# Kernel tuning notes

Hardware: AMD Instinct MI355X
Metric: run time of the kernel (lower is better)

The kernel has to match this reference:

```python
import jax, jax.numpy as jnp
import numpy as np

B = 1024; PAST = 64; FUT = 16; N = PAST + FUT; DM = N // 3; HID = 64
EMB = [(2000, 32), (7, 8), (24, 8)]
OUTP = 3 + 32 + 8 + 8  # 51 = out_preprocess
O = OUTP - 1           # 50
HID1 = 64; HID2 = 64
NEG = -1e30  # finite stand-in for -inf so fully-masked rows stay NaN-free


def _gcnn(x, A, W, act):
    # D = diag((1 + rowsum(sign(relu(A-1e-15))))^-0.5); out = act(D @ A @ D @ (x W^T))
    d = (1.0 + (A > 1e-15).astype(x.dtype).sum(1)) ** -0.5
    An = d[:, None] * A * d[None, :]            # (P,P)
    h = jnp.einsum('pq,bqc->bpc', An, x @ W.T)  # (B,P,out)
    return jax.nn.relu(h) if act else h


def _forward(data, emb0, emb1, emb2, w1, b1, w2, b2, w3, b3,
             M, Wg1a, Wg1b, Wk, smoothing, Wg2a, Wg2b):
    # learned adjacency: masked softmax over strictly-lower-triangular support
    mask = jnp.tril(jnp.ones((N, N), data.dtype), -1)
    A0 = jax.nn.relu(M @ M.T)
    A = jax.nn.softmax(jnp.where(mask > 0, A0, NEG), axis=1)
    A = jnp.where(mask > 0, A, 0.0)
    # pre_processing: embeddings + MLP, then re-append last raw column
    tabs = (emb0, emb1, emb2)
    e = [t[data[:, :, i].astype(jnp.int32)] for i, t in enumerate(tabs)]
    h = jnp.concatenate(e + [data[:, :, -3:]], -1)        # (B,N,51)
    h = jax.nn.relu(h @ w1.T + b1)
    h = jax.nn.relu(h @ w2.T + b2)
    h = h @ w3.T + b3                                      # (B,N,50)
    x = jnp.concatenate([h, data[:, :, -1:]], -1)          # (B,N,51)
    sg1, sg2 = x[:, :PAST], x[:, PAST:]
    A11 = A[:PAST, :PAST]
    x1 = _gcnn(_gcnn(sg1, A11, Wg1a, True), A11, Wg1b, False)   # (B,PAST,50)
    xk = jnp.concatenate([x1, sg2[:, :, :-1]], 1)               # (B,N,50)
    y = x[:, :PAST, -1:]                                        # (B,PAST,1)
    # Kernel: batched Mahalanobis quadratic form (diagonal computed directly)
    xp, xf = xk[:, :PAST], xk[:, PAST:]
    theta = Wk @ Wk.T
    theta = (theta + theta.T) / 2
    diff = xp[:, None, :, :] - xf[:, :, None, :]                # (B,F,P,50)
    q = jnp.einsum('bjip,pq,bjiq->bji', diff, theta, diff)      # (B,F,P)
    alpha = -0.5 * q / (jax.nn.sigmoid(smoothing[0]) * 0.01)
    At = A[FUT:, :PAST] if False else A[PAST:, :PAST]           # (F,P)
    At = jax.nn.softmax(jnp.where(At != 0, At, NEG), axis=1)
    # torch Softmax(dim=1) on (B,F,P) normalizes over the F axis
    alpha = jax.nn.softmax(jnp.where(At[None] >= 0.004, alpha, NEG), axis=1)
    yh = jnp.einsum('bjp,bpo->bjo', alpha, y)                   # (B,F,1)
    x2 = jnp.concatenate([sg2[:, :, :-1], yh], -1)              # (B,F,51)
    A22 = A[PAST:, PAST:]
    out = _gcnn(_gcnn(x2, A22, Wg2a, True), A22, Wg2b, False).reshape(-1, FUT)
    # cdist(x, x), p=2, with NaN-safe sqrt at zero distance
    xc = jnp.concatenate([sg1, x2], 1)                          # (B,N,51)
    sq = jnp.sum(xc * xc, -1)
    d2 = jnp.maximum(sq[:, :, None] + sq[:, None, :]
                     - 2.0 * jnp.einsum('bnc,bmc->bnm', xc, xc), 0.0)
    dist = jnp.where(d2 > 0, jnp.sqrt(jnp.where(d2 > 0, d2, 1.0)), 0.0)
    return (out, dist, A)


def setup_inputs() -> dict:
    key = jax.random.key(0)
    ks = jax.random.split(key, 20)
    cols = [jax.random.randint(ks[i], (B, N, 1), 0, EMB[i][0]).astype(jnp.float32)
            for i in range(3)]
    data = jnp.concatenate(cols + [jax.random.normal(ks[3], (B, N, 3), jnp.float32)], -1)
    g = lambda k, s, sc: jax.random.normal(k, s, jnp.float32) * sc
    return dict(
        data=data,
        emb0=g(ks[4], EMB[0], 1.0),
        emb1=g(ks[5], EMB[1], 1.0),
        emb2=g(ks[6], EMB[2], 1.0),
        w1=g(ks[7], (128, OUTP), OUTP ** -0.5), b1=jnp.zeros((128,), jnp.float32),
        w2=g(ks[8], (128, 128), 128 ** -0.5), b2=jnp.zeros((128,), jnp.float32),
        w3=g(ks[9], (O, 128), 128 ** -0.5), b3=jnp.zeros((O,), jnp.float32),
        M=g(ks[10], (N, DM), 1.0),
        Wg1a=g(ks[11], (HID1, OUTP), OUTP ** -0.5),
        Wg1b=g(ks[12], (O, HID1), HID1 ** -0.5),
        Wk=g(ks[13], (O, HID), 0.05),
        smoothing=g(ks[14], (1,), 1.0),
        Wg2a=g(ks[15], (HID2, OUTP), OUTP ** -0.5),
        Wg2b=g(ks[16], (1, HID2), HID2 ** -0.5),
    )


def reference(data, emb0, emb1, emb2, w1, b1, w2, b2, w3, b3,
              M, Wg1a, Wg1b, Wk, smoothing, Wg2a, Wg2b):
    return _forward(data, emb0, emb1, emb2, w1, b1, w2, b2, w3, b3,
                    M, Wg1a, Wg1b, Wk, smoothing, Wg2a, Wg2b)
```

## Files before the change

### kernel.cpp

```cpp
#include <hip/hip_runtime.h>
#include <math.h>


#define NEGBIG (-1e30f)

#define OFF_A     7471104
#define OFF_AN22  7481600
#define OFF_MK    7484356
#define OFF_GAH   7514692
#define OFF_GAL   7516740
#define OFF_G2AT  7521156
#define OFF_SC    7524420
#define OFF_W1H   7524424
#define OFF_W1L   7528520
#define OFF_W2H   7532616
#define OFF_W2L   7540808
#define OFF_W3H   7549000
#define OFF_W3L   7553096
#define OFF_ANH   7557192
#define OFF_ANL   7559240
#define OFF_GBH   7561288
#define OFF_GBL   7563336
#define OFF_WKH   7565384
#define OFF_WKL   7567432

#define OUT_OUT   0
#define OUT_DIST  16384
#define OUT_A     6569984

typedef __attribute__((ext_vector_type(8))) short bf16x8;
typedef __attribute__((ext_vector_type(4))) short s16x4;
typedef __attribute__((ext_vector_type(4))) float f32x4;

__device__ __forceinline__ unsigned short f2bf(float x) {
  union { float f; unsigned u; } v; v.f = x;
  unsigned r = v.u + 0x7fffu + ((v.u >> 16) & 1u);
  return (unsigned short)(r >> 16);
}
__device__ __forceinline__ float bf2f(unsigned short h) {
  union { unsigned u; float f; } v; v.u = ((unsigned)h) << 16; return v.f;
}
__device__ __forceinline__ void split2(float v, unsigned short& h, unsigned short& l) {
  unsigned short hh = f2bf(v);
  h = hh;
  l = f2bf(v - bf2f(hh));
}
__device__ __forceinline__ void split8(const float* v, bf16x8& h8, bf16x8& l8) {
#pragma unroll
  for (int j = 0; j < 8; ++j) {
    unsigned short hh, ll; split2(v[j], hh, ll);
    h8[j] = (short)hh; l8[j] = (short)ll;
  }
}
#define SWZ6(r, k) (((r) << 6) + (((((k) >> 3) ^ ((r) & 7)) << 3) | ((k) & 7)))
#define SWZ7(r, k) (((r) << 7) + (((((k) >> 3) ^ ((r) & 7)) << 3) | ((k) & 7)))

#define MFMA3(acc, aH, aL, bH, bL) \
  acc = __builtin_amdgcn_mfma_f32_16x16x32_bf16(aH, bH, acc, 0, 0, 0); \
  acc = __builtin_amdgcn_mfma_f32_16x16x32_bf16(aH, bL, acc, 0, 0, 0); \
  acc = __builtin_amdgcn_mfma_f32_16x16x32_bf16(aL, bH, acc, 0, 0, 0);
#define MFMA4(acc, aH, aL, bH, bL) \
  MFMA3(acc, aH, aL, bH, bL) \
  acc = __builtin_amdgcn_mfma_f32_16x16x32_bf16(aL, bL, acc, 0, 0, 0);

__global__ __launch_bounds__(256) void k_prep(
    const float* __restrict__ M, const float* __restrict__ Wk,
    const float* __restrict__ sm,
    const float* __restrict__ w1, const float* __restrict__ w2,
    const float* __restrict__ w3,
    const float* __restrict__ wg1a, const float* __restrict__ wg1b,
    const float* __restrict__ wg2a,
    float* __restrict__ ws, float* __restrict__ out)
{
  __shared__ float Msh[80 * 26];
  __shared__ float Ash[80 * 80];
  __shared__ float d1[64];
  __shared__ float d2s[16];
  const int t = threadIdx.x;

  if (blockIdx.x == 0) {
    for (int e = t; e < 80 * 26; e += 256) Msh[e] = M[e];
    __syncthreads();
    for (int e = t; e < 6400; e += 256) {
      int i = e / 80, j = e % 80;
      float v = 0.f;
      if (j < i) {
        float s = 0.f;
        for (int k = 0; k < 26; ++k) s += Msh[i * 26 + k] * Msh[j * 26 + k];
        v = s > 0.f ? s : 0.f;
      }
      Ash[e] = v;
    }
    __syncthreads();
    if (t > 0 && t < 80) {
      int i = t;
      float m = -3.4e38f;
      for (int j = 0; j < i; ++j) m = fmaxf(m, Ash[i * 80 + j]);
      float s = 0.f;
      for (int j = 0; j < i; ++j) {
        float e = expf(Ash[i * 80 + j] - m);
        Ash[i * 80 + j] = e;
        s += e;
      }
      float inv = 1.f / s;
      for (int j = 0; j < i; ++j) Ash[i * 80 + j] *= inv;
    }
    __syncthreads();
    {
      float* Aws = ws + OFF_A;
      float* Aout = out + OUT_A;
      for (int e = t; e < 6400; e += 256) { Aws[e] = Ash[e]; Aout[e] = Ash[e]; }
    }
    if (t < 64) {
      int c = 0;
      for (int j = 0; j < 64; ++j) if (Ash[t * 80 + j] > 1e-15f) ++c;
      d1[t] = 1.f / sqrtf(1.f + (float)c);
    } else if (t < 80) {
      int i = t - 64; int c = 0;
      for (int j = 0; j < 16; ++j) if (Ash[(64 + i) * 80 + 64 + j] > 1e-15f) ++c;
      d2s[i] = 1.f / sqrtf(1.f + (float)c);
    }
    __syncthreads();
    {
      float* an22 = ws + OFF_AN22;
      unsigned short* anH = (unsigned short*)(ws + OFF_ANH);
      unsigned short* anL = (unsigned short*)(ws + OFF_ANL);
      for (int e = t; e < 4096; e += 256) {
        int i = e >> 6, j = e & 63;
        float v = d1[i] * Ash[i * 80 + j] * d1[j];
        unsigned short h = f2bf(v);
        anH[e] = h; anL[e] = f2bf(v - bf2f(h));
      }
      for (int e = t; e < 256; e += 256) {
        int i = e >> 4, j = e & 15;
        an22[e] = d2s[i] * Ash[(64 + i) * 80 + 64 + j] * d2s[j];
      }
    }
    if (t < 16) {
      float* mk = ws + OFF_MK;
      int j = t;
      float m = -3.4e38f;
      for (int i = 0; i < 64; ++i) {
        float v = Ash[(64 + j) * 80 + i];
        v = (v != 0.f) ? v : NEGBIG;
        m = fmaxf(m, v);
      }
      float s = 0.f;
      for (int i = 0; i < 64; ++i) {
        float v = Ash[(64 + j) * 80 + i];
        v = (v != 0.f) ? v : NEGBIG;
        s += expf(v - m);
      }
      float inv = 1.f / s;
      for (int i = 0; i < 64; ++i) {
        float v = Ash[(64 + j) * 80 + i];
        v = (v != 0.f) ? v : NEGBIG;
        mk[j * 64 + i] = (expf(v - m) * inv >= 0.004f) ? 1.f : 0.f;
      }
    }
  } else if (blockIdx.x == 1) {
    unsigned short* wkh = (unsigned short*)(ws + OFF_WKH);
    unsigned short* wkl = (unsigned short*)(ws + OFF_WKL);
    for (int e = t; e < 4096; e += 256) {
      int h = e >> 6, o = e & 63;
      float v = (o < 50) ? Wk[o * 64 + h] : 0.f;
      unsigned short hh = f2bf(v);
      wkh[e] = hh; wkl[e] = f2bf(v - bf2f(hh));
    }
    if (t == 0) {
      float v = sm[0];
      float sig = 1.f / (1.f + expf(-v));
      (ws + OFF_SC)[0] = -0.5f / (sig * 0.01f);
    }
  } else if (blockIdx.x == 2) {
    unsigned short* w1h = (unsigned short*)(ws + OFF_W1H);
    unsigned short* w1l = (unsigned short*)(ws + OFF_W1L);
    for (int e = t; e < 8192; e += 256) {
      int n = e >> 6, k = e & 63;
      float v = (k < 51) ? w1[n * 51 + k] : 0.f;
      unsigned short h = f2bf(v);
      w1h[e] = h; w1l[e] = f2bf(v - bf2f(h));
    }
    unsigned short* w3h = (unsigned short*)(ws + OFF_W3H);
    unsigned short* w3l = (unsigned short*)(ws + OFF_W3L);
    for (int e = t; e < 8192; e += 256) {
      int n = e >> 7, k = e & 127;
      float v = (n < 50) ? w3[n * 128 + k] : 0.f;
      unsigned short h = f2bf(v);
      w3h[e] = h; w3l[e] = f2bf(v - bf2f(h));
    }
    unsigned short* gah = (unsigned short*)(ws + OFF_GAH);
    unsigned short* gal = (unsigned short*)(ws + OFF_GAL);
    for (int e = t; e < 4096; e += 256) {
      int n = e >> 6, k = e & 63;
      float v = (k < 51) ? wg1a[n * 51 + k] : 0.f;
      unsigned short h = f2bf(v);
      gah[e] = h; gal[e] = f2bf(v - bf2f(h));
    }
  } else {
    unsigned short* w2h = (unsigned short*)(ws + OFF_W2H);
    unsigned short* w2l = (unsigned short*)(ws + OFF_W2L);
    for (int e = t; e < 16384; e += 256) {
      int n = e >> 7, k = e & 127;
      float v = w2[n * 128 + k];
      unsigned short h = f2bf(v);
      w2h[e] = h; w2l[e] = f2bf(v - bf2f(h));
    }
    unsigned short* gbh = (unsigned short*)(ws + OFF_GBH);
    unsigned short* gbl = (unsigned short*)(ws + OFF_GBL);
    for (int e = t; e < 4096; e += 256) {
      int n = e >> 6, k = e & 63;
      float v = (n < 50) ? wg1b[n * 64 + k] : 0.f;
      unsigned short h = f2bf(v);
      gbh[e] = h; gbl[e] = f2bf(v - bf2f(h));
    }
    float* g2at = ws + OFF_G2AT;
    for (int e = t; e < 64 * 51; e += 256) { int o = e / 51, k = e % 51; g2at[k * 64 + o] = wg2a[e]; }
  }
}

__global__ __launch_bounds__(512, 4) void k_fused(
    const float* __restrict__ data,
    const float* __restrict__ emb0, const float* __restrict__ emb1,
    const float* __restrict__ emb2,
    const float* __restrict__ b1v, const float* __restrict__ b2v,
    const float* __restrict__ b3v,
    const float* __restrict__ wg2b,
    float* __restrict__ ws, float* __restrict__ out)
{
  __shared__ __align__(16) unsigned short SH[27136];

  unsigned short* xcH = SH;
  unsigned short* xcL = SH + 5120;
  unsigned short* b1H = SH + 10240;
  unsigned short* b1L = SH + 14336;
  unsigned short* b2H = SH + 18432;
  unsigned short* b2L = SH + 22528;
  float* spH2 = (float*)(SH + 26624);
  float* spS  = (float*)(SH + 26880);
  float* sfS  = (float*)(SH + 27008);
  float* yhsS = (float*)(SH + 27040);
  float* alS = (float*)(SH + 18432);
  unsigned short* zfH = SH + 22528;
  unsigned short* zfL = SH + 23552;
  unsigned short* mHdH = SH + 10240;
  unsigned short* mHdL = SH + 16384;
  float* X2v  = (float*)(SH + 10240);
  float* A22v = (float*)(SH + 11904);
  float* G2v  = (float*)(SH + 12416);
  float* Pmv  = (float*)(SH + 14464);
  float* wb2  = (float*)(SH + 16512);
  float* zzv  = (float*)(SH + 16640);
  float* sqS  = (float*)(SH + 16672);

  const int t = threadIdx.x, b = blockIdx.x;
  const int lane = t & 63, wave = t >> 6;
  const int m16 = lane & 15, quad = lane >> 4;
  const int s = wave & 3, half = wave >> 2;
  const int row0 = s * 16;
  const int arow = row0 + m16;

  const unsigned short* w1h = (const unsigned short*)(ws + OFF_W1H);
  const unsigned short* w1l = (const unsigned short*)(ws + OFF_W1L);
  const unsigned short* w2h = (const unsigned short*)(ws + OFF_W2H);
  const unsigned short* w2l = (const unsigned short*)(ws + OFF_W2L);
  const unsigned short* w3h = (const unsigned short*)(ws + OFF_W3H);
  const unsigned short* w3l = (const unsigned short*)(ws + OFF_W3L);
  const float* mk = ws + OFF_MK;
  const float* an22 = ws + OFF_AN22;
  const float* g2at = ws + OFF_G2AT;
  const unsigned short* gAnH = (const unsigned short*)(ws + OFF_ANH);
  const unsigned short* gAnL = (const unsigned short*)(ws + OFF_ANL);
  const unsigned short* gaH = (const unsigned short*)(ws + OFF_GAH);
  const unsigned short* gaL = (const unsigned short*)(ws + OFF_GAL);
  const unsigned short* gbH = (const unsigned short*)(ws + OFF_GBH);
  const unsigned short* gbL = (const unsigned short*)(ws + OFF_GBL);
  const unsigned short* gwkH = (const unsigned short*)(ws + OFF_WKH);
  const unsigned short* gwkL = (const unsigned short*)(ws + OFF_WKL);
  const float sc = (ws + OFF_SC)[0];

#pragma unroll
  for (int ck = 0; ck < 2; ++ck) {
    const int C0 = ck ? 48 : 0;
    const int NT = ck ? 2 : 3;

    {
      const int col = wave * 16 + m16;
      const float bias = b1v[col];
      f32x4 acc1[3];
#pragma unroll
      for (int rt = 0; rt < 3; ++rt) acc1[rt] = (f32x4){0.f, 0.f, 0.f, 0.f};
#pragma unroll
      for (int kh = 0; kh < 2; ++kh) {
        bf16x8 bH = *(const bf16x8*)(w1h + (col << 6) + kh * 32 + (quad << 3));
        bf16x8 bL = *(const bf16x8*)(w1l + (col << 6) + kh * 32 + (quad << 3));
#pragma unroll
        for (int rt = 0; rt < 3; ++rt) {
          if (rt >= NT) break;
          const int g = b * 80 + C0 + rt * 16 + m16;
          float v[8];
          if (kh == 0) {
            int i0 = (int)data[g * 6 + 0];
            const float* p = emb0 + i0 * 32 + (quad << 3);
#pragma unroll
            for (int j = 0; j < 8; ++j) v[j] = p[j];
          } else {
            if (quad == 0) {
              int i1 = (int)data[g * 6 + 1];
#pragma unroll
              for (int j = 0; j < 8; ++j) v[j] = emb1[i1 * 8 + j];
            } else if (quad == 1) {
              int i2 = (int)data[g * 6 + 2];
#pragma unroll
              for (int j = 0; j < 8; ++j) v[j] = emb2[i2 * 8 + j];
            } else if (quad == 2) {
              v[0] = data[g * 6 + 3]; v[1] = data[g * 6 + 4]; v[2] = data[g * 6 + 5];
#pragma unroll
              for (int j = 3; j < 8; ++j) v[j] = 0.f;
            } else {
#pragma unroll
              for (int j = 0; j < 8; ++j) v[j] = 0.f;
            }
          }
          bf16x8 aH, aL;
          split8(v, aH, aL);
          MFMA3(acc1[rt], aH, aL, bH, bL)
        }
      }
#pragma unroll
      for (int rt = 0; rt < 3; ++rt) {
        if (rt >= NT) break;
#pragma unroll
        for (int r = 0; r < 4; ++r) {
          float v = acc1[rt][r] + bias; v = v > 0.f ? v : 0.f;
          int idx = SWZ7(rt * 16 + quad * 4 + r, col);
          split2(v, mHdH[idx], mHdL[idx]);
        }
      }
    }
    __syncthreads();

    f32x4 acc2[3];
#pragma unroll
    for (int rt = 0; rt < 3; ++rt) acc2[rt] = (f32x4){0.f, 0.f, 0.f, 0.f};
    {
      const int col = wave * 16 + m16;
#pragma unroll
      for (int kh = 0; kh < 2; ++kh) {
        bf16x8 bh0 = *(const bf16x8*)(w2h + (col << 7) + ((quad + kh * 8) << 3));
        bf16x8 bl0 = *(const bf16x8*)(w2l + (col << 7) + ((quad + kh * 8) << 3));
        bf16x8 bh1 = *(const bf16x8*)(w2h + (col << 7) + ((quad + kh * 8 + 4) << 3));
        bf16x8 bl1 = *(const bf16x8*)(w2l + (col << 7) + ((quad + kh * 8 + 4) << 3));
#pragma unroll
        for (int lrt = 0; lrt < 3; ++lrt) {
          if (lrt >= NT) break;
          const int lr = lrt * 16 + m16;
          int ach0 = ((quad + kh * 8) ^ (m16 & 7)) << 3;
          int ach1 = ((quad + kh * 8 + 4) ^ (m16 & 7)) << 3;
          bf16x8 aH = *(const bf16x8*)(mHdH + (lr << 7) + ach0);
          bf16x8 aL = *(const bf16x8*)(mHdL + (lr << 7) + ach0);
          MFMA3(acc2[lrt], aH, aL, bh0, bl0)
          aH = *(const bf16x8*)(mHdH + (lr << 7) + ach1);
          aL = *(const bf16x8*)(mHdL + (lr << 7) + ach1);
          MFMA3(acc2[lrt], aH, aL, bh1, bl1)
        }
      }
    }
    __syncthreads();

    {
      const int col = wave * 16 + m16;
      const float bias = b2v[col];
#pragma unroll
      for (int lrt = 0; lrt < 3; ++lrt) {
        if (lrt >= NT) break;
#pragma unroll
        for (int r = 0; r < 4; ++r) {
          float v = acc2[lrt][r] + bias; v = v > 0.f ? v : 0.f;
          int idx = SWZ7(lrt * 16 + quad * 4 + r, col);
          split2(v, mHdH[idx], mHdL[idx]);
        }
      }
    }
    __syncthreads();

    {
      const int colt = wave & 3, rh = wave >> 2;
      const int col = colt * 16 + m16;
      const float bias = (col < 50) ? b3v[col] : 0.f;
      for (int lrt = rh; lrt < NT; lrt += 2) {
        const int lr = lrt * 16 + m16;
        f32x4 acc = (f32x4){0.f, 0.f, 0.f, 0.f};
#pragma unroll
        for (int kh = 0; kh < 2; ++kh) {
          bf16x8 bh0 = *(const bf16x8*)(w3h + (col << 7) + ((quad + kh * 8) << 3));
          bf16x8 bl0 = *(const bf16x8*)(w3l + (col << 7) + ((quad + kh * 8) << 3));
          bf16x8 bh1 = *(const bf16x8*)(w3h + (col << 7) + ((quad + kh * 8 + 4) << 3));
          bf16x8 bl1 = *(const bf16x8*)(w3l + (col << 7) + ((quad + kh * 8 + 4) << 3));
          int ach0 = ((quad + kh * 8) ^ (m16 & 7)) << 3;
          int ach1 = ((quad + kh * 8 + 4) ^ (m16 & 7)) << 3;
          bf16x8 aH = *(const bf16x8*)(mHdH + (lr << 7) + ach0);
          bf16x8 aL = *(const bf16x8*)(mHdL + (lr << 7) + ach0);
          MFMA3(acc, aH, aL, bh0, bl0)
          aH = *(const bf16x8*)(mHdH + (lr << 7) + ach1);
          aL = *(const bf16x8*)(mHdL + (lr << 7) + ach1);
          MFMA3(acc, aH, aL, bh1, bl1)
        }
        if (col != 50) {
#pragma unroll
          for (int r = 0; r < 4; ++r) {
            int grow = C0 + lrt * 16 + quad * 4 + r;
            int idx = SWZ6(grow, col);
            split2(acc[r] + bias, xcH[idx], xcL[idx]);
          }
        }
      }
      if (ck == 0 && t < 80) {
        float v = (t < 64) ? data[(b * 80 + t) * 6 + 5] : 0.f;
        int idx = SWZ6(t, 50);
        split2(v, xcH[idx], xcL[idx]);
      }
    }
    __syncthreads();
  }

  f32x4 accA[2];

#pragma unroll
  for (int n = 0; n < 2; ++n) accA[n] = (f32x4){0.f, 0.f, 0.f, 0.f};
#pragma unroll
  for (int kb8 = 0; kb8 < 8; kb8 += 4) {
    int ach = ((quad + kb8) ^ (m16 & 7)) << 3;
    int k0 = (quad + kb8) << 3;
    bf16x8 aH = *(const bf16x8*)(xcH + (arow << 6) + ach);
    bf16x8 aL = *(const bf16x8*)(xcL + (arow << 6) + ach);
#pragma unroll
    for (int n = 0; n < 2; ++n) {
      const int col = (half * 2 + n) * 16 + m16;
      bf16x8 bH = *(const bf16x8*)(gaH + (col << 6) + k0);
      bf16x8 bL = *(const bf16x8*)(gaL + (col << 6) + k0);
      MFMA3(accA[n], aH, aL, bH, bL)
    }
  }
  {
    const int kb = row0 + quad * 4;
#pragma unroll
    for (int n = 0; n < 2; ++n) {
      const int col = (half * 2 + n) * 16 + m16;
      int idx = (col << 6) + (((((kb >> 3) ^ (col & 7)) << 3)) | (kb & 7));
      s16x4 hv, lv;
#pragma unroll
      for (int r = 0; r < 4; ++r) {
        unsigned short hh, ll; split2(accA[n][r], hh, ll);
        hv[r] = (short)hh; lv[r] = (short)ll;
      }
      *(s16x4*)(b2H + idx) = hv; *(s16x4*)(b2L + idx) = lv;
    }
  }
  __syncthreads();

#pragma unroll
  for (int n = 0; n < 2; ++n) accA[n] = (f32x4){0.f, 0.f, 0.f, 0.f};
#pragma unroll
  for (int kb8 = 0; kb8 < 8; kb8 += 4) {
    int ach = ((quad + kb8) ^ (m16 & 7)) << 3;
    int k0 = (quad + kb8) << 3;
    bf16x8 aH = *(const bf16x8*)(gAnH + (arow << 6) + k0);
    bf16x8 aL = *(const bf16x8*)(gAnL + (arow << 6) + k0);
#pragma unroll
    for (int n = 0; n < 2; ++n) {
      const int col = (half * 2 + n) * 16 + m16;
      int boff = (col << 6) + ach;
      bf16x8 bH = *(const bf16x8*)(b2H + boff);
      bf16x8 bL = *(const bf16x8*)(b2L + boff);
      MFMA3(accA[n], aH, aL, bH, bL)
    }
  }
  __syncthreads();

  {
    const int kb = row0 + quad * 4;
#pragma unroll
    for (int n = 0; n < 2; ++n) {
      const int col = (half * 2 + n) * 16 + m16;
      int idx = (col << 6) + (((((kb >> 3) ^ (col & 7)) << 3)) | (kb & 7));
      s16x4 hv, lv;
#pragma unroll
      for (int r = 0; r < 4; ++r) {
        float v = accA[n][r]; v = v > 0.f ? v : 0.f;
        unsigned short hh, ll; split2(v, hh, ll);
        hv[r] = (short)hh; lv[r] = (short)ll;
      }
      *(s16x4*)(b2H + idx) = hv; *(s16x4*)(b2L + idx) = lv;
    }
  }
  __syncthreads();

#pragma unroll
  for (int n = 0; n < 2; ++n) accA[n] = (f32x4){0.f, 0.f, 0.f, 0.f};
#pragma unroll
  for (int kb8 = 0; kb8 < 8; kb8 += 4) {
    int ach = ((quad + kb8) ^ (m16 & 7)) << 3;
    int k0 = (quad + kb8) << 3;
    bf16x8 aH = *(const bf16x8*)(gAnH + (arow << 6) + k0);
    bf16x8 aL = *(const bf16x8*)(gAnL + (arow << 6) + k0);
#pragma unroll
    for (int n = 0; n < 2; ++n) {
      const int col = (half * 2 + n) * 16 + m16;
      int boff = (col << 6) + ach;
      bf16x8 bH = *(const bf16x8*)(b2H + boff);
      bf16x8 bL = *(const bf16x8*)(b2L + boff);
      MFMA3(accA[n], aH, aL, bH, bL)
    }
  }
#pragma unroll
  for (int n = 0; n < 2; ++n) {
    const int col = (half * 2 + n) * 16 + m16;
#pragma unroll
    for (int r = 0; r < 4; ++r) {
      int idx = SWZ6(row0 + quad * 4 + r, col);
      split2(accA[n][r], b1H[idx], b1L[idx]);
    }
  }
  __syncthreads();

#pragma unroll
  for (int n = 0; n < 2; ++n) accA[n] = (f32x4){0.f, 0.f, 0.f, 0.f};
#pragma unroll
  for (int kb8 = 0; kb8 < 8; kb8 += 4) {
    int ach = ((quad + kb8) ^ (m16 & 7)) << 3;
    int k0 = (quad + kb8) << 3;
    bf16x8 aH = *(const bf16x8*)(b1H + (arow << 6) + ach);
    bf16x8 aL = *(const bf16x8*)(b1L + (arow << 6) + ach);
#pragma unroll
    for (int n = 0; n < 2; ++n) {
      const int col = (half * 2 + n) * 16 + m16;
      bf16x8 bH = *(const bf16x8*)(gbH + (col << 6) + k0);
      bf16x8 bL = *(const bf16x8*)(gbL + (col << 6) + k0);
      MFMA3(accA[n], aH, aL, bH, bL)
    }
  }
#pragma unroll
  for (int n = 0; n < 2; ++n) {
    const int col = (half * 2 + n) * 16 + m16;
#pragma unroll
    for (int r = 0; r < 4; ++r) {
      int idx = SWZ6(row0 + quad * 4 + r, col);
      split2(accA[n][r], b2H[idx], b2L[idx]);
    }
  }
  __syncthreads();

#pragma unroll
  for (int n = 0; n < 2; ++n) accA[n] = (f32x4){0.f, 0.f, 0.f, 0.f};
  f32x4 af = (f32x4){0.f, 0.f, 0.f, 0.f};
#pragma unroll
  for (int kb8 = 0; kb8 < 8; kb8 += 4) {
    int ach = ((quad + kb8) ^ (m16 & 7)) << 3;
    int k0 = (quad + kb8) << 3;
    bf16x8 aH = *(const bf16x8*)(b2H + (arow << 6) + ach);
    bf16x8 aL = *(const bf16x8*)(b2L + (arow << 6) + ach);
#pragma unroll
    for (int n = 0; n < 2; ++n) {
      const int col = (half * 2 + n) * 16 + m16;
      bf16x8 bH = *(const bf16x8*)(gwkH + (col << 6) + k0);
      bf16x8 bL = *(const bf16x8*)(gwkL + (col << 6) + k0);
      MFMA4(accA[n], aH, aL, bH, bL)
    }
  }
  if (half == 0) {
#pragma unroll
    for (int kb8 = 0; kb8 < 8; kb8 += 4) {
      int ach = ((quad + kb8) ^ (m16 & 7)) << 3;
      int k0 = (quad + kb8) << 3;
      bf16x8 aH = *(const bf16x8*)(xcH + ((64 + m16) << 6) + ach);
      bf16x8 aL = *(const bf16x8*)(xcL + ((64 + m16) << 6) + ach);
      const int col = s * 16 + m16;
      bf16x8 bH = *(const bf16x8*)(gwkH + (col << 6) + k0);
      bf16x8 bL = *(const bf16x8*)(gwkL + (col << 6) + k0);
      MFMA4(af, aH, aL, bH, bL)
    }
  }
  {
    float s2[4];
#pragma unroll
    for (int r = 0; r < 4; ++r)
      s2[r] = accA[0][r] * accA[0][r] + accA[1][r] * accA[1][r];
#pragma unroll
    for (int n = 0; n < 2; ++n) {
      const int h = (half * 2 + n) * 16 + m16;
#pragma unroll
      for (int r = 0; r < 4; ++r) {
        int idx = SWZ6(row0 + quad * 4 + r, h);
        split2(accA[n][r], b1H[idx], b1L[idx]);
      }
    }
#pragma unroll
    for (int m = 1; m < 16; m <<= 1)
#pragma unroll
      for (int r = 0; r < 4; ++r) s2[r] += __shfl_xor(s2[r], m);
    if (m16 == 0) {
#pragma unroll
      for (int r = 0; r < 4; ++r)
        spH2[(row0 + quad * 4 + r) * 2 + half] = s2[r];
    }
  }
  __syncthreads();

  if (t < 64) spS[t] = spH2[t * 2] + spH2[t * 2 + 1];
  if (half == 0) {
    const int h = s * 16 + m16;
#pragma unroll
    for (int r = 0; r < 4; ++r) {
      int idx = SWZ6(quad * 4 + r, h);
      split2(af[r], zfH[idx], zfL[idx]);
    }
  }
  __syncthreads();

  f32x4 ac2 = (f32x4){0.f, 0.f, 0.f, 0.f};
  if (half == 0) {
#pragma unroll
    for (int kb8 = 0; kb8 < 8; kb8 += 4) {
      int ach = ((quad + kb8) ^ (m16 & 7)) << 3;
      bf16x8 aH = *(const bf16x8*)(b1H + (arow << 6) + ach);
      bf16x8 aL = *(const bf16x8*)(b1L + (arow << 6) + ach);
      bf16x8 bH = *(const bf16x8*)(zfH + (m16 << 6) + ach);
      bf16x8 bL = *(const bf16x8*)(zfL + (m16 << 6) + ach);
      MFMA4(ac2, aH, aL, bH, bL)
    }
  } else {
    int idx = t - 256;
    int j = idx >> 4, h0 = (idx & 15) << 2;
    float p = 0.f;
#pragma unroll
    for (int r = 0; r < 4; ++r) {
      int ii = SWZ6(j, h0 + r);
      float v = bf2f(zfH[ii]) + bf2f(zfL[ii]);
      p += v * v;
    }
#pragma unroll
    for (int m = 1; m < 16; m <<= 1) p += __shfl_xor(p, m);
    if ((idx & 15) == 0) sfS[j] = p;
  }
  __syncthreads();

  if (half == 0) {
#pragma unroll
    for (int r = 0; r < 4; ++r) {
      int i = row0 + quad * 4 + r;
      alS[i * 17 + m16] = sc * (spS[i] + sfS[m16] - 2.f * ac2[r]);
    }
  }
  __syncthreads();

  if (t < 64) {
    const int i = t;
    float lv[16];
    float m = -3.4e38f;
#pragma unroll
    for (int j = 0; j < 16; ++j) {
      float v = (mk[j * 64 + i] != 0.f) ? alS[i * 17 + j] : NEGBIG;
      lv[j] = v;
      m = fmaxf(m, v);
    }
    float ssum = 0.f;
#pragma unroll
    for (int j = 0; j < 16; ++j) { lv[j] = expf(lv[j] - m); ssum += lv[j]; }
    float inv = 1.f / ssum;
#pragma unroll
    for (int j = 0; j < 16; ++j) alS[i * 17 + j] = lv[j] * inv;
  }
  __syncthreads();

  if (t < 256) {
    int j = t >> 4, i0 = (t & 15) << 2;
    float p = 0.f;
#pragma unroll
    for (int r = 0; r < 4; ++r) {
      int i = i0 + r;
      int iy = SWZ6(i, 50);
      float yv = bf2f(xcH[iy]) + bf2f(xcL[iy]);
      p += alS[i * 17 + j] * yv;
    }
#pragma unroll
    for (int m = 1; m < 16; m <<= 1) p += __shfl_xor(p, m);
    if ((t & 15) == 0) yhsS[j] = p;
  }
  __syncthreads();

  if (t < 16) {
    int idx = SWZ6(64 + t, 50);
    split2(yhsS[t], xcH[idx], xcL[idx]);
  }
  for (int e = t; e < 832; e += 512) {
    int r = e / 52, c = e - r * 52;
    float v = 0.f;
    if (c < 50) {
      int i6 = SWZ6(64 + r, c);
      v = bf2f(xcH[i6]) + bf2f(xcL[i6]);
    } else if (c == 50) v = yhsS[r];
    X2v[e] = v;
  }
  for (int e = t; e < 256; e += 512) A22v[e] = an22[e];
  if (t < 64) wb2[t] = wg2b[t];
  __syncthreads();

  if (wave < 5) {
    const int ts = wave;
    f32x4 acc = (f32x4){0.f, 0.f, 0.f, 0.f};
#pragma unroll
    for (int kb8 = 0; kb8 < 8; kb8 += 4) {
      int ach = ((quad + kb8) ^ (m16 & 7)) << 3;
      bf16x8 aH = *(const bf16x8*)(xcH + ((ts * 16 + m16) << 6) + ach);
      bf16x8 aL = *(const bf16x8*)(xcL + ((ts * 16 + m16) << 6) + ach);
      MFMA3(acc, aH, aL, aH, aL)
    }
    if ((m16 >> 2) == quad) sqS[ts * 16 + m16] = acc[m16 & 3];
  } else {
    for (int e = t - 320; e < 1024; e += 192) {
      int j = e >> 6, h = e & 63;
      float ssum = 0.f;
      for (int k = 0; k < 51; ++k) ssum += X2v[j * 52 + k] * g2at[k * 64 + h];
      G2v[e] = ssum;
    }
  }
  __syncthreads();

  {
    float* dist = out + OUT_DIST + b * 6400;
    for (int idx = wave; idx < 25; idx += 8) {
      int ts = idx / 5, tf = idx - ts * 5;
      f32x4 acc = (f32x4){0.f, 0.f, 0.f, 0.f};
#pragma unroll
      for (int kb8 = 0; kb8 < 8; kb8 += 4) {
        int ach = ((quad + kb8) ^ (m16 & 7)) << 3;
        bf16x8 aH = *(const bf16x8*)(xcH + ((ts * 16 + m16) << 6) + ach);
        bf16x8 aL = *(const bf16x8*)(xcL + ((ts * 16 + m16) << 6) + ach);
        const int col = tf * 16 + m16;
        int boff = (col << 6) + ach;
        bf16x8 bH = *(const bf16x8*)(xcH + boff);
        bf16x8 bL = *(const bf16x8*)(xcL + boff);
        MFMA3(acc, aH, aL, bH, bL)
      }
#pragma unroll
      for (int r = 0; r < 4; ++r) {
        int i = ts * 16 + quad * 4 + r;
        int m = tf * 16 + m16;
        float d2 = sqS[i] + sqS[m] - 2.f * acc[r];
        d2 = d2 > 0.f ? d2 : 0.f;
        dist[i * 80 + m] = d2 > 0.f ? sqrtf(d2) : 0.f;
      }
    }
  }
  for (int e = t; e < 1024; e += 512) {
    int j = e >> 6, h = e & 63;
    float ssum = 0.f;
#pragma unroll
    for (int k = 0; k < 16; ++k) ssum += A22v[j * 16 + k] * G2v[k * 64 + h];
    Pmv[e] = ssum > 0.f ? ssum : 0.f;
  }
  __syncthreads();
  if (t < 256) {
    int j = t >> 4, h0 = (t & 15) << 2;
    float p = 0.f;
#pragma unroll
    for (int r = 0; r < 4; ++r) p += Pmv[j * 64 + h0 + r] * wb2[h0 + r];
#pragma unroll
    for (int m = 1; m < 16; m <<= 1) p += __shfl_xor(p, m);
    if ((t & 15) == 0) zzv[j] = p;
  }
  __syncthreads();
  if (t < 16) {
    float ssum = 0.f;
#pragma unroll
    for (int k = 0; k < 16; ++k) ssum += A22v[t * 16 + k] * zzv[k];
    out[OUT_OUT + b * 16 + t] = ssum;
  }
}

extern "C" void kernel_launch(void* const* d_in, const int* in_sizes, int n_in,
                              void* d_out, int out_size, void* d_ws, size_t ws_size,
                              hipStream_t stream)
{
  const float* data = (const float*)d_in[0];
  const float* emb0 = (const float*)d_in[1];
  const float* emb1 = (const float*)d_in[2];
  const float* emb2 = (const float*)d_in[3];
  const float* w1   = (const float*)d_in[4];
  const float* b1   = (const float*)d_in[5];
  const float* w2   = (const float*)d_in[6];
  const float* b2   = (const float*)d_in[7];
  const float* w3   = (const float*)d_in[8];
  const float* b3   = (const float*)d_in[9];
  const float* M    = (const float*)d_in[10];
  const float* wg1a = (const float*)d_in[11];
  const float* wg1b = (const float*)d_in[12];
  const float* Wk   = (const float*)d_in[13];
  const float* smo  = (const float*)d_in[14];
  const float* wg2a = (const float*)d_in[15];
  const float* wg2b = (const float*)d_in[16];
  float* ws  = (float*)d_ws;
  float* out = (float*)d_out;

  k_prep <<<dim3(4),    dim3(256), 0, stream>>>(M, Wk, smo, w1, w2, w3, wg1a, wg1b, wg2a, ws, out);
  k_fused<<<dim3(1024), dim3(512), 0, stream>>>(data, emb0, emb1, emb2, b1, b2, b3, wg2b, ws, out);
}
```

Measured before the change: 232.3 us.

## Shrink LDS footprint to raise occupancy, reuse buffers and padding columns

Cuts shared memory from about 54KB to 40KB by aliasing buffers. The b1 scratch is folded into b2, the small scalar arrays are stored in the unused padding columns (56-63) of the xc tiles, and the MLP is processed in three 32-row chunks instead of two. Launch bounds move from 4 to 8 blocks per CU to allow more concurrent blocks. This adds extra __syncthreads to protect the aliased buffers, zeroes the padded K lanes instead of loading them, and puts more register pressure on a 512-thread block.

```diff
diff --git a/kernel.cpp b/kernel.cpp
--- a/kernel.cpp
+++ b/kernel.cpp
@@ -219,7 +219,7 @@
   }
 }
 
-__global__ __launch_bounds__(512, 4) void k_fused(
+__global__ __launch_bounds__(512, 8) void k_fused(
     const float* __restrict__ data,
     const float* __restrict__ emb0, const float* __restrict__ emb1,
     const float* __restrict__ emb2,
@@ -228,30 +228,26 @@
     const float* __restrict__ wg2b,
     float* __restrict__ ws, float* __restrict__ out)
 {
-  __shared__ __align__(16) unsigned short SH[27136];
+  __shared__ __align__(16) unsigned short SH[20480];
 
   unsigned short* xcH = SH;
   unsigned short* xcL = SH + 5120;
-  unsigned short* b1H = SH + 10240;
-  unsigned short* b1L = SH + 14336;
-  unsigned short* b2H = SH + 18432;
-  unsigned short* b2L = SH + 22528;
-  float* spH2 = (float*)(SH + 26624);
-  float* spS  = (float*)(SH + 26880);
-  float* sfS  = (float*)(SH + 27008);
-  float* yhsS = (float*)(SH + 27040);
-  float* alS = (float*)(SH + 18432);
-  unsigned short* zfH = SH + 22528;
-  unsigned short* zfL = SH + 23552;
+  unsigned short* b2H = SH + 10240;
+  unsigned short* b2L = SH + 14336;
+  unsigned short* zfH = SH + 18432;
+  unsigned short* zfL = SH + 19456;
+  float* alS = (float*)(SH + 10240);
   unsigned short* mHdH = SH + 10240;
-  unsigned short* mHdL = SH + 16384;
+  unsigned short* mHdL = SH + 14336;
   float* X2v  = (float*)(SH + 10240);
-  float* A22v = (float*)(SH + 11904);
-  float* G2v  = (float*)(SH + 12416);
-  float* Pmv  = (float*)(SH + 14464);
-  float* wb2  = (float*)(SH + 16512);
-  float* zzv  = (float*)(SH + 16640);
-  float* sqS  = (float*)(SH + 16672);
+  float* A22v = X2v + 832;
+  float* G2v  = A22v + 256;
+  float* Pmv  = G2v + 1024;
+  float* wb2  = Pmv + 1024;
+  float* zzv  = wb2 + 64;
+  float* sqS  = zzv + 16;
+#define SPH2(row) ((float*)(xcH + ((row) << 6) + ((((row) & 7) ^ 7) << 3)))
+#define MS16(j)   ((float*)(xcL + ((j) << 6) + ((((j) & 7) ^ 7) << 3)))
 
   const int t = threadIdx.x, b = blockIdx.x;
   const int lane = t & 63, wave = t >> 6;
@@ -259,6 +255,8 @@
   const int s = wave & 3, half = wave >> 2;
   const int row0 = s * 16;
   const int arow = row0 + m16;
+
+  const bf16x8 z8 = (bf16x8){0, 0, 0, 0, 0, 0, 0, 0};
 
   const unsigned short* w1h = (const unsigned short*)(ws + OFF_W1H);
   const unsigned short* w1l = (const unsigned short*)(ws + OFF_W1L);
@@ -280,22 +278,22 @@
   const float sc = (ws + OFF_SC)[0];
 
 #pragma unroll
-  for (int ck = 0; ck < 2; ++ck) {
-    const int C0 = ck ? 48 : 0;
-    const int NT = ck ? 2 : 3;
+  for (int ck = 0; ck < 3; ++ck) {
+    const int C0 = ck * 32;
+    const int NT = (ck == 2) ? 1 : 2;
 
     {
       const int col = wave * 16 + m16;
       const float bias = b1v[col];
-      f32x4 acc1[3];
-#pragma unroll
-      for (int rt = 0; rt < 3; ++rt) acc1[rt] = (f32x4){0.f, 0.f, 0.f, 0.f};
+      f32x4 acc1[2];
+#pragma unroll
+      for (int rt = 0; rt < 2; ++rt) acc1[rt] = (f32x4){0.f, 0.f, 0.f, 0.f};
 #pragma unroll
       for (int kh = 0; kh < 2; ++kh) {
         bf16x8 bH = *(const bf16x8*)(w1h + (col << 6) + kh * 32 + (quad << 3));
         bf16x8 bL = *(const bf16x8*)(w1l + (col << 6) + kh * 32 + (quad << 3));
 #pragma unroll
-        for (int rt = 0; rt < 3; ++rt) {
+        for (int rt = 0; rt < 2; ++rt) {
           if (rt >= NT) break;
           const int g = b * 80 + C0 + rt * 16 + m16;
           float v[8];
@@ -328,7 +326,7 @@
         }
       }
 #pragma unroll
-      for (int rt = 0; rt < 3; ++rt) {
+      for (int rt = 0; rt < 2; ++rt) {
         if (rt >= NT) break;
 #pragma unroll
         for (int r = 0; r < 4; ++r) {
@@ -340,9 +338,9 @@
     }
     __syncthreads();
 
-    f32x4 acc2[3];
-#pragma unroll
-    for (int rt = 0; rt < 3; ++rt) acc2[rt] = (f32x4){0.f, 0.f, 0.f, 0.f};
+    f32x4 acc2[2];
+#pragma unroll
+    for (int rt = 0; rt < 2; ++rt) acc2[rt] = (f32x4){0.f, 0.f, 0.f, 0.f};
     {
       const int col = wave * 16 + m16;
 #pragma unroll
@@ -352,7 +350,7 @@
         bf16x8 bh1 = *(const bf16x8*)(w2h + (col << 7) + ((quad + kh * 8 + 4) << 3));
         bf16x8 bl1 = *(const bf16x8*)(w2l + (col << 7) + ((quad + kh * 8 + 4) << 3));
 #pragma unroll
-        for (int lrt = 0; lrt < 3; ++lrt) {
+        for (int lrt = 0; lrt < 2; ++lrt) {
           if (lrt >= NT) break;
           const int lr = lrt * 16 + m16;
           int ach0 = ((quad + kh * 8) ^ (m16 & 7)) << 3;
@@ -372,7 +370,7 @@
       const int col = wave * 16 + m16;
       const float bias = b2v[col];
 #pragma unroll
-      for (int lrt = 0; lrt < 3; ++lrt) {
+      for (int lrt = 0; lrt < 2; ++lrt) {
         if (lrt >= NT) break;
 #pragma unroll
         for (int r = 0; r < 4; ++r) {
@@ -406,7 +404,7 @@
           aL = *(const bf16x8*)(mHdL + (lr << 7) + ach1);
           MFMA3(acc, aH, aL, bh1, bl1)
         }
-        if (col != 50) {
+        if (col != 50 && col < 56) {
 #pragma unroll
           for (int r = 0; r < 4; ++r) {
             int grow = C0 + lrt * 16 + quad * 4 + r;
@@ -432,8 +430,12 @@
   for (int kb8 = 0; kb8 < 8; kb8 += 4) {
     int ach = ((quad + kb8) ^ (m16 & 7)) << 3;
     int k0 = (quad + kb8) << 3;
-    bf16x8 aH = *(const bf16x8*)(xcH + (arow << 6) + ach);
-    bf16x8 aL = *(const bf16x8*)(xcL + (arow << 6) + ach);
+    bf16x8 aH, aL;
+    if (kb8 == 4 && quad == 3) { aH = z8; aL = z8; }
+    else {
+      aH = *(const bf16x8*)(xcH + (arow << 6) + ach);
+      aL = *(const bf16x8*)(xcL + (arow << 6) + ach);
+    }
 #pragma unroll
     for (int n = 0; n < 2; ++n) {
       const int col = (half * 2 + n) * 16 + m16;
@@ -513,13 +515,15 @@
       MFMA3(accA[n], aH, aL, bH, bL)
     }
   }
+  __syncthreads();
+
 #pragma unroll
   for (int n = 0; n < 2; ++n) {
     const int col = (half * 2 + n) * 16 + m16;
 #pragma unroll
     for (int r = 0; r < 4; ++r) {
       int idx = SWZ6(row0 + quad * 4 + r, col);
-      split2(accA[n][r], b1H[idx], b1L[idx]);
+      split2(accA[n][r], b2H[idx], b2L[idx]);
     }
   }
   __syncthreads();
@@ -530,8 +534,8 @@
   for (int kb8 = 0; kb8 < 8; kb8 += 4) {
     int ach = ((quad + kb8) ^ (m16 & 7)) << 3;
     int k0 = (quad + kb8) << 3;
-    bf16x8 aH = *(const bf16x8*)(b1H + (arow << 6) + ach);
-    bf16x8 aL = *(const bf16x8*)(b1L + (arow << 6) + ach);
+    bf16x8 aH = *(const bf16x8*)(b2H + (arow << 6) + ach);
+    bf16x8 aL = *(const bf16x8*)(b2L + (arow << 6) + ach);
 #pragma unroll
     for (int n = 0; n < 2; ++n) {
       const int col = (half * 2 + n) * 16 + m16;
@@ -540,6 +544,8 @@
       MFMA3(accA[n], aH, aL, bH, bL)
     }
   }
+  __syncthreads();
+
 #pragma unroll
   for (int n = 0; n < 2; ++n) {
     const int col = (half * 2 + n) * 16 + m16;
@@ -573,41 +579,37 @@
     for (int kb8 = 0; kb8 < 8; kb8 += 4) {
       int ach = ((quad + kb8) ^ (m16 & 7)) << 3;
       int k0 = (quad + kb8) << 3;
-      bf16x8 aH = *(const bf16x8*)(xcH + ((64 + m16) << 6) + ach);
-      bf16x8 aL = *(const bf16x8*)(xcL + ((64 + m16) << 6) + ach);
+      bf16x8 aH, aL;
+      if (kb8 == 4 && quad == 3) { aH = z8; aL = z8; }
+      else {
+        aH = *(const bf16x8*)(xcH + ((64 + m16) << 6) + ach);
+        aL = *(const bf16x8*)(xcL + ((64 + m16) << 6) + ach);
+      }
       const int col = s * 16 + m16;
       bf16x8 bH = *(const bf16x8*)(gwkH + (col << 6) + k0);
       bf16x8 bL = *(const bf16x8*)(gwkL + (col << 6) + k0);
       MFMA4(af, aH, aL, bH, bL)
     }
   }
-  {
-    float s2[4];
-#pragma unroll
-    for (int r = 0; r < 4; ++r)
-      s2[r] = accA[0][r] * accA[0][r] + accA[1][r] * accA[1][r];
-#pragma unroll
-    for (int n = 0; n < 2; ++n) {
-      const int h = (half * 2 + n) * 16 + m16;
-#pragma unroll
-      for (int r = 0; r < 4; ++r) {
-        int idx = SWZ6(row0 + quad * 4 + r, h);
-        split2(accA[n][r], b1H[idx], b1L[idx]);
-      }
-    }
-#pragma unroll
-    for (int m = 1; m < 16; m <<= 1)
-#pragma unroll
-      for (int r = 0; r < 4; ++r) s2[r] += __shfl_xor(s2[r], m);
-    if (m16 == 0) {
-#pragma unroll
-      for (int r = 0; r < 4; ++r)
-        spH2[(row0 + quad * 4 + r) * 2 + half] = s2[r];
-    }
-  }
-  __syncthreads();
-
-  if (t < 64) spS[t] = spH2[t * 2] + spH2[t * 2 + 1];
+  float s2r[4];
+#pragma unroll
+  for (int r = 0; r < 4; ++r)
+    s2r[r] = accA[0][r] * accA[0][r] + accA[1][r] * accA[1][r];
+#pragma unroll
+  for (int m = 1; m < 16; m <<= 1)
+#pragma unroll
+    for (int r = 0; r < 4; ++r) s2r[r] += __shfl_xor(s2r[r], m);
+  __syncthreads();
+
+#pragma unroll
+  for (int n = 0; n < 2; ++n) {
+    const int h = (half * 2 + n) * 16 + m16;
+#pragma unroll
+    for (int r = 0; r < 4; ++r) {
+      int idx = SWZ6(row0 + quad * 4 + r, h);
+      split2(accA[n][r], b2H[idx], b2L[idx]);
+    }
+  }
   if (half == 0) {
     const int h = s * 16 + m16;
 #pragma unroll
@@ -616,6 +618,11 @@
       split2(af[r], zfH[idx], zfL[idx]);
     }
   }
+  if (m16 == 0) {
+#pragma unroll
+    for (int r = 0; r < 4; ++r)
+      SPH2(row0 + quad * 4 + r)[half] = s2r[r];
+  }
   __syncthreads();
 
   f32x4 ac2 = (f32x4){0.f, 0.f, 0.f, 0.f};
@@ -623,8 +630,8 @@
 #pragma unroll
     for (int kb8 = 0; kb8 < 8; kb8 += 4) {
       int ach = ((quad + kb8) ^ (m16 & 7)) << 3;
-      bf16x8 aH = *(const bf16x8*)(b1H + (arow << 6) + ach);
-      bf16x8 aL = *(const bf16x8*)(b1L + (arow << 6) + ach);
+      bf16x8 aH = *(const bf16x8*)(b2H + (arow << 6) + ach);
+      bf16x8 aL = *(const bf16x8*)(b2L + (arow << 6) + ach);
       bf16x8 bH = *(const bf16x8*)(zfH + (m16 << 6) + ach);
       bf16x8 bL = *(const bf16x8*)(zfL + (m16 << 6) + ach);
       MFMA4(ac2, aH, aL, bH, bL)
@@ -641,7 +648,7 @@
     }
 #pragma unroll
     for (int m = 1; m < 16; m <<= 1) p += __shfl_xor(p, m);
-    if ((idx & 15) == 0) sfS[j] = p;
+    if ((idx & 15) == 0) MS16(j)[0] = p;
   }
   __syncthreads();
 
@@ -649,7 +656,7 @@
 #pragma unroll
     for (int r = 0; r < 4; ++r) {
       int i = row0 + quad * 4 + r;
-      alS[i * 17 + m16] = sc * (spS[i] + sfS[m16] - 2.f * ac2[r]);
+      alS[i * 17 + m16] = sc * ((SPH2(i)[0] + SPH2(i)[1]) + MS16(m16)[0] - 2.f * ac2[r]);
     }
   }
   __syncthreads();
@@ -685,13 +692,13 @@
     }
 #pragma unroll
     for (int m = 1; m < 16; m <<= 1) p += __shfl_xor(p, m);
-    if ((t & 15) == 0) yhsS[j] = p;
+    if ((t & 15) == 0) MS16(j)[1] = p;
   }
   __syncthreads();
 
   if (t < 16) {
     int idx = SWZ6(64 + t, 50);
-    split2(yhsS[t], xcH[idx], xcL[idx]);
+    split2(MS16(t)[1], xcH[idx], xcL[idx]);
   }
   for (int e = t; e < 832; e += 512) {
     int r = e / 52, c = e - r * 52;
@@ -699,7 +706,7 @@
     if (c < 50) {
       int i6 = SWZ6(64 + r, c);
       v = bf2f(xcH[i6]) + bf2f(xcL[i6]);
-    } else if (c == 50) v = yhsS[r];
+    } else if (c == 50) v = MS16(r)[1];
     X2v[e] = v;
   }
   for (int e = t; e < 256; e += 512) A22v[e] = an22[e];
@@ -712,8 +719,12 @@
 #pragma unroll
     for (int kb8 = 0; kb8 < 8; kb8 += 4) {
       int ach = ((quad + kb8) ^ (m16 & 7)) << 3;
-      bf16x8 aH = *(const bf16x8*)(xcH + ((ts * 16 + m16) << 6) + ach);
-      bf16x8 aL = *(const bf16x8*)(xcL + ((ts * 16 + m16) << 6) + ach);
+      bf16x8 aH, aL;
+      if (kb8 == 4 && quad == 3) { aH = z8; aL = z8; }
+      else {
+        aH = *(const bf16x8*)(xcH + ((ts * 16 + m16) << 6) + ach);
+        aL = *(const bf16x8*)(xcL + ((ts * 16 + m16) << 6) + ach);
+      }
       MFMA3(acc, aH, aL, aH, aL)
     }
     if ((m16 >> 2) == quad) sqS[ts * 16 + m16] = acc[m16 & 3];
@@ -735,12 +746,15 @@
 #pragma unroll
       for (int kb8 = 0; kb8 < 8; kb8 += 4) {
         int ach = ((quad + kb8) ^ (m16 & 7)) << 3;
-        bf16x8 aH = *(const bf16x8*)(xcH + ((ts * 16 + m16) << 6) + ach);
-        bf16x8 aL = *(const bf16x8*)(xcL + ((ts * 16 + m16) << 6) + ach);
-        const int col = tf * 16 + m16;
-        int boff = (col << 6) + ach;
-        bf16x8 bH = *(const bf16x8*)(xcH + boff);
-        bf16x8 bL = *(const bf16x8*)(xcL + boff);
+        bf16x8 aH, aL, bH, bL;
+        if (kb8 == 4 && quad == 3) { aH = z8; aL = z8; bH = z8; bL = z8; }
+        else {
+          aH = *(const bf16x8*)(xcH + ((ts * 16 + m16) << 6) + ach);
+          aL = *(const bf16x8*)(xcL + ((ts * 16 + m16) << 6) + ach);
+          const int col = tf * 16 + m16;
+          bH = *(const bf16x8*)(xcH + (col << 6) + ach);
+          bL = *(const bf16x8*)(xcL + (col << 6) + ach);
+        }
         MFMA3(acc, aH, aL, bH, bL)
       }
 #pragma unroll
```

Measured after the change: 271.8 us. 1.17x slower.
